# Optimization experiments

Hardware: AMD Instinct MI355X
Metric: run time of the kernel (lower is better)

## Reference

```python
import jax, jax.numpy as jnp
import numpy as np

T, B, E, H = 512, 128, 512, 512
MEM, CTX = 500, 300

def setup_inputs() -> dict:
    key = jax.random.key(0)
    ks = jax.random.split(key, 16)
    s = 0.05
    return {
        "input_seqs": jax.random.normal(ks[0], (B, T, E), jnp.float32),
        "input_lengths": jax.random.randint(ks[1], (B,), 1, T + 1),
        "Wih_f": jax.random.normal(ks[2], (4 * H, E + CTX), jnp.float32) * s,
        "Whh_f": jax.random.normal(ks[3], (4 * H, H), jnp.float32) * s,
        "bih_f": jax.random.normal(ks[4], (4 * H,), jnp.float32) * s,
        "bhh_f": jax.random.normal(ks[5], (4 * H,), jnp.float32) * s,
        "Wih_b": jax.random.normal(ks[6], (4 * H, E + CTX), jnp.float32) * s,
        "Whh_b": jax.random.normal(ks[7], (4 * H, H), jnp.float32) * s,
        "bih_b": jax.random.normal(ks[8], (4 * H,), jnp.float32) * s,
        "bhh_b": jax.random.normal(ks[9], (4 * H,), jnp.float32) * s,
        "Mk_f": jax.random.normal(ks[10], (MEM, H), jnp.float32) * s,
        "Mv_f": jax.random.normal(ks[11], (CTX, MEM), jnp.float32) * s,
        "Mk_b": jax.random.normal(ks[12], (MEM, H), jnp.float32) * s,
        "Mv_b": jax.random.normal(ks[13], (CTX, MEM), jnp.float32) * s,
    }

def _mem_ctx(h, Mk, Mv):
    # exp-key softmax read: exp(h Mk^T) normalized by row sum, then project to CTX
    a = jnp.exp(h @ Mk.T)                      # [B, MEM]
    return (a / jnp.sum(a, axis=-1, keepdims=True)) @ Mv.T  # [B, CTX]

def _cell(x, h, c, Wih, Whh, b):
    g = x @ Wih.T + h @ Whh.T + b              # [B, 4H], gate order i,f,g,o
    i, f, gg, o = jnp.split(g, 4, axis=-1)
    c = jax.nn.sigmoid(f) * c + jax.nn.sigmoid(i) * jnp.tanh(gg)
    return jax.nn.sigmoid(o) * jnp.tanh(c), c

def reference(input_seqs, input_lengths, Wih_f, Whh_f, bih_f, bhh_f,
              Wih_b, Whh_b, bih_b, bhh_b, Mk_f, Mv_f, Mk_b, Mv_b):
    xs = jnp.transpose(input_seqs, (1, 0, 2))          # [T, B, E]
    dt = xs.dtype
    mask = (jnp.arange(T)[:, None] < input_lengths[None, :]).astype(dt)[:, :, None]  # [T,B,1]
    b_f = bih_f + bhh_f
    b_b = bih_b + bhh_b
    z = jnp.zeros((B, H), dt)
    zf = jnp.zeros((), dt)
    one = jnp.ones((), dt)

    def fstep(carry, x):
        h, c, flag = carry
        ctx = flag * _mem_ctx(h, Mk_f, Mv_f)           # step 0 uses zero dummy context
        h, c = _cell(jnp.concatenate([x, ctx], -1), h, c, Wih_f, Whh_f, b_f)
        return (h, c, one), h
    _, f_hs = jax.lax.scan(fstep, (z, z, zf), xs)      # [T, B, H] per-step hidden

    def bstep(carry, xm):
        x, m = xm
        hm, h, c, flag = carry
        ctx = flag * _mem_ctx(hm, Mk_b, Mv_b)
        h, c = _cell(jnp.concatenate([x, ctx], -1), h, c, Wih_b, Whh_b, b_b)
        return (h * m, h, c, one), None                # masked hidden feeds next memory read
    (h_b, _, _, _), _ = jax.lax.scan(bstep, (z, z, z, zf), (xs[::-1], mask[::-1]))

    idx = jnp.clip(input_lengths - 1, 0, T - 1)
    h_f = f_hs[idx, jnp.arange(B)]                     # final valid forward hidden per example
    # permute(1,2,0).view(B,-1): interleave fwd/bwd per hidden unit
    return jnp.stack([h_f, h_b], axis=-1).reshape(B, 2 * H)
```

## Files before the change

### kernel.cpp

```cpp
#include <hip/hip_runtime.h>
#include <hip/hip_bf16.h>

#define T_   512
#define B_   128
#define E_   512
#define H_   512
#define G4_  2048
#define MEM_ 500
#define CTX_ 300
#define EC_  (E_ + CTX_)
#define SPIN_MAX 65536

typedef short sh8  __attribute__((ext_vector_type(8)));
typedef float f32x4 __attribute__((ext_vector_type(4)));

struct ScanParams {
  const float* __restrict__ x;
  const short* __restrict__ xbf;
  const int*   __restrict__ len;
  const float* __restrict__ Wih0; const float* __restrict__ Whh0;
  const float* __restrict__ bih0; const float* __restrict__ bhh0;
  const float* __restrict__ Wih1; const float* __restrict__ Whh1;
  const float* __restrict__ bih1; const float* __restrict__ bhh1;
  const float* __restrict__ Mk0;  const float* __restrict__ Mk1;
  const float* __restrict__ Mf;
  short* __restrict__ hbf;
  short* __restrict__ aB;
  unsigned* __restrict__ bar;
  float* __restrict__ out;
};

__device__ __forceinline__ float sigm_(float x) { return 1.f / (1.f + __expf(-x)); }
__device__ __forceinline__ float tanh_(float x) { return 1.f - 2.f / (__expf(2.f * x) + 1.f); }
__device__ __forceinline__ short f2bs(float f) {
  __hip_bfloat16 h = __float2bfloat16(f);
  short s; __builtin_memcpy(&s, &h, 2); return s;
}
__device__ __forceinline__ float bs2f(short s) {
  unsigned u = ((unsigned)(unsigned short)s) << 16;
  float f; __builtin_memcpy(&f, &u, 4); return f;
}

struct F16 { sh8 v[16]; };
__device__ __forceinline__ void gld16(F16& f, const short* base) {
  asm volatile(
      "global_load_dwordx4 %0, %16, off sc1\n\t"
      "global_load_dwordx4 %1, %16, off offset:64 sc1\n\t"
      "global_load_dwordx4 %2, %16, off offset:128 sc1\n\t"
      "global_load_dwordx4 %3, %16, off offset:192 sc1\n\t"
      "global_load_dwordx4 %4, %16, off offset:256 sc1\n\t"
      "global_load_dwordx4 %5, %16, off offset:320 sc1\n\t"
      "global_load_dwordx4 %6, %16, off offset:384 sc1\n\t"
      "global_load_dwordx4 %7, %16, off offset:448 sc1\n\t"
      "global_load_dwordx4 %8, %16, off offset:512 sc1\n\t"
      "global_load_dwordx4 %9, %16, off offset:576 sc1\n\t"
      "global_load_dwordx4 %10, %16, off offset:640 sc1\n\t"
      "global_load_dwordx4 %11, %16, off offset:704 sc1\n\t"
      "global_load_dwordx4 %12, %16, off offset:768 sc1\n\t"
      "global_load_dwordx4 %13, %16, off offset:832 sc1\n\t"
      "global_load_dwordx4 %14, %16, off offset:896 sc1\n\t"
      "global_load_dwordx4 %15, %16, off offset:960 sc1\n\t"
      "s_waitcnt vmcnt(0)"
      : "=&v"(f.v[0]), "=&v"(f.v[1]), "=&v"(f.v[2]), "=&v"(f.v[3]),
        "=&v"(f.v[4]), "=&v"(f.v[5]), "=&v"(f.v[6]), "=&v"(f.v[7]),
        "=&v"(f.v[8]), "=&v"(f.v[9]), "=&v"(f.v[10]), "=&v"(f.v[11]),
        "=&v"(f.v[12]), "=&v"(f.v[13]), "=&v"(f.v[14]), "=&v"(f.v[15])
      : "v"(base)
      : "memory");
}

__device__ __forceinline__ void st4s(short* base, unsigned d0, unsigned d1,
                                     unsigned d2, unsigned d3) {
  asm volatile(
      "global_store_short %4, %0, off sc1\n\t"
      "global_store_short %4, %1, off offset:1024 sc1\n\t"
      "global_store_short %4, %2, off offset:2048 sc1\n\t"
      "global_store_short %4, %3, off offset:3072 sc1\n\t"
      "s_waitcnt vmcnt(0)"
      :: "v"(d0), "v"(d1), "v"(d2), "v"(d3), "v"(base) : "memory");
}

__device__ __forceinline__ void st8s(short* base, const unsigned* d) {
  asm volatile(
      "global_store_short %8, %0, off sc1\n\t"
      "global_store_short %8, %1, off offset:1024 sc1\n\t"
      "global_store_short %8, %2, off offset:2048 sc1\n\t"
      "global_store_short %8, %3, off offset:3072 sc1\n\t"
      "global_store_short %8, %4, off offset:8 sc1\n\t"
      "global_store_short %8, %5, off offset:1032 sc1\n\t"
      "global_store_short %8, %6, off offset:2056 sc1\n\t"
      "global_store_short %8, %7, off offset:3080 sc1"
      :: "v"(d[0]), "v"(d[1]), "v"(d[2]), "v"(d[3]),
         "v"(d[4]), "v"(d[5]), "v"(d[6]), "v"(d[7]), "v"(base) : "memory");
}

__device__ __forceinline__ bool hchk(const unsigned* hflW, unsigned ep, int lane) {
  unsigned v = __hip_atomic_load(&hflW[lane], __ATOMIC_RELAXED, __HIP_MEMORY_SCOPE_AGENT);
  return __all((int)(v >= ep));
}
__device__ __forceinline__ bool achk(const unsigned* aflW, unsigned ep, int lane) {
  unsigned v = __hip_atomic_load(&aflW[lane & 31], __ATOMIC_RELAXED, __HIP_MEMORY_SCOPE_AGENT);
  return __all((int)(v >= ep));
}
__device__ __forceinline__ void spin_h(const unsigned* hflW, unsigned ep, int lane) {
  int n = 0;
  while (!hchk(hflW, ep, lane) && n < SPIN_MAX) { __builtin_amdgcn_s_sleep(1); ++n; }
}
__device__ __forceinline__ void spin_a(const unsigned* aflW, unsigned ep, int lane) {
  int n = 0;
  while (!achk(aflW, ep, lane) && n < SPIN_MAX) { __builtin_amdgcn_s_sleep(1); ++n; }
}
__device__ __forceinline__ void fset(unsigned* slot, unsigned ep, int lane) {
  if (lane == 0)
    __hip_atomic_store(slot, ep, __ATOMIC_RELAXED, __HIP_MEMORY_SCOPE_AGENT);
}

__global__ __launch_bounds__(256) void xcvt_kernel(const float* __restrict__ x,
                                                   short* __restrict__ xbf) {
  const size_t i = ((size_t)blockIdx.x * 256 + threadIdx.x) * 8;
  f32x4 a = *reinterpret_cast<const f32x4*>(x + i);
  f32x4 b = *reinterpret_cast<const f32x4*>(x + i + 4);
  sh8 v;
  #pragma unroll
  for (int j = 0; j < 4; ++j) { v[j] = f2bs(a[j]); v[4 + j] = f2bs(b[j]); }
  *reinterpret_cast<sh8*>(xbf + i) = v;
}

__global__ __launch_bounds__(256) void mfused_kernel(
    const float* __restrict__ WihF, const float* __restrict__ WihB,
    const float* __restrict__ MvF,  const float* __restrict__ MvB,
    float* __restrict__ Mf) {
  const int d  = blockIdx.x >> 7;
  const int j0 = (blockIdx.x & 127) * 16;
  const float* __restrict__ Wih = d ? WihB : WihF;
  const float* __restrict__ Mv  = d ? MvB  : MvF;
  __shared__ float Wl[16][CTX_ + 1];
  for (int i = threadIdx.x; i < 16 * CTX_; i += 256) {
    int r = i / CTX_, cc = i - r * CTX_;
    Wl[r][cc] = Wih[(size_t)(j0 + r) * EC_ + E_ + cc];
  }
  __syncthreads();
  const int jj = threadIdx.x & 15;
  for (int m = threadIdx.x >> 4; m < MEM_; m += 16) {
    float acc = 0.f;
    for (int cc = 0; cc < CTX_; ++cc)
      acc = fmaf(Mv[cc * MEM_ + m], Wl[jj][cc], acc);
    Mf[(size_t)d * MEM_ * G4_ + (size_t)m * G4_ + j0 + jj] = acc;
  }
}

__global__ __launch_bounds__(512, 1) void scan_kernel(ScanParams p) {
  const int dir  = blockIdx.x >> 6;
  const int w    = blockIdx.x & 63;
  const int tid  = threadIdx.x;
  const int wv   = tid >> 6;
  const int lane = tid & 63;

  __shared__ __align__(16) short WgL[32 * 2 * 64 * 8];
  __shared__ __align__(16) short MkL[16 * 64 * 8];
  __shared__ __align__(16) short MfL[16 * 2 * 64 * 8];
  __shared__ int LvL[B_];

  const float* __restrict__ Wihd = dir ? p.Wih1 : p.Wih0;
  const float* __restrict__ Whhd = dir ? p.Whh1 : p.Whh0;
  const float* __restrict__ bihd = dir ? p.bih1 : p.bih0;
  const float* __restrict__ bhhd = dir ? p.bhh1 : p.bhh0;
  const float* __restrict__ Mkd  = dir ? p.Mk1  : p.Mk0;
  const float* __restrict__ Mfd  = p.Mf + (size_t)dir * MEM_ * G4_;
  short* __restrict__ aBd = p.aB + (size_t)dir * B_ * 512;

  unsigned* __restrict__ hflW = p.bar + (size_t)(dir * 8 + wv) * 64;
  unsigned* __restrict__ aflW = p.bar + 1024 + (size_t)(dir * 8 + wv) * 32;

  const int  ct   = w >> 1;
  const bool prod = ((wv >> 2) == (w & 1));

  for (int i = tid; i < 32 * 2 * 64; i += 512) {
    const int ks = i >> 7, r2 = i & 127, ct2 = r2 >> 6, l2 = r2 & 63;
    const int col = l2 & 15, kg = l2 >> 4;
    const int k0 = ks * 32 + kg * 8;
    const int gc = (col & 3) * H_ + 8 * w + 4 * ct2 + (col >> 2);
    const float* src = (k0 < E_) ? (Wihd + (size_t)gc * EC_ + k0)
                                 : (Whhd + (size_t)gc * H_ + (k0 - E_));
    sh8 v;
    #pragma unroll
    for (int j = 0; j < 8; ++j) v[j] = f2bs(src[j]);
    *reinterpret_cast<sh8*>(&WgL[i * 8]) = v;
  }
  for (int i = tid; i < 16 * 64; i += 512) {
    const int ks = i >> 6, l2 = i & 63;
    const int col = l2 & 15, kg = l2 >> 4;
    const int k0 = ks * 32 + kg * 8;
    const int mr = 16 * ct + col;
    sh8 v;
    #pragma unroll
    for (int j = 0; j < 8; ++j)
      v[j] = (mr < MEM_) ? f2bs(Mkd[(size_t)mr * H_ + k0 + j]) : (short)0;
    *reinterpret_cast<sh8*>(&MkL[i * 8]) = v;
  }
  for (int i = tid; i < 16 * 2 * 64; i += 512) {
    const int ks = i >> 7, r2 = i & 127, ct2 = r2 >> 6, l2 = r2 & 63;
    const int col = l2 & 15, kg = l2 >> 4;
    const int gc = (col & 3) * H_ + 8 * w + 4 * ct2 + (col >> 2);
    const int m0 = ks * 32 + kg * 8;
    sh8 v;
    #pragma unroll
    for (int j = 0; j < 8; ++j)
      v[j] = (m0 + j < MEM_) ? f2bs(Mfd[(size_t)(m0 + j) * G4_ + gc]) : (short)0;
    *reinterpret_cast<sh8*>(&MfL[i * 8]) = v;
  }
  if (tid < B_) LvL[tid] = p.len[tid];

  const int cc  = lane & 15;
  const int q   = cc & 3;
  const int uu  = cc >> 2;
  const int kg8 = (lane >> 4) * 8;
  const int arow = lane & 15;
  float biasl[2];
  #pragma unroll
  for (int ct2 = 0; ct2 < 2; ++ct2) {
    const int gc = q * H_ + 8 * w + 4 * ct2 + uu;
    biasl[ct2] = bihd[gc] + bhhd[gc];
  }

  float creg[2][4] = {{0.f,0.f,0.f,0.f},{0.f,0.f,0.f,0.f}};
  __syncthreads();

  const int mylen = LvL[16 * wv + arow];

  auto xhalf = [&](int t, f32x4* acc) {
    if (p.xbf) {
      const short* xb = p.xbf + ((size_t)(16 * wv + arow) * T_ + t) * E_ + kg8;
      for (int ks = 0; ks < 16; ++ks) {
        sh8 af = *reinterpret_cast<const sh8*>(xb + ks * 32);
        acc[0] = __builtin_amdgcn_mfma_f32_16x16x32_bf16(
            af, *reinterpret_cast<const sh8*>(&WgL[((ks * 2 + 0) * 64 + lane) * 8]), acc[0], 0, 0, 0);
        acc[1] = __builtin_amdgcn_mfma_f32_16x16x32_bf16(
            af, *reinterpret_cast<const sh8*>(&WgL[((ks * 2 + 1) * 64 + lane) * 8]), acc[1], 0, 0, 0);
      }
    } else {
      const float* xp0 = p.x + ((size_t)(16 * wv + arow) * T_ + t) * E_ + kg8;
      for (int ks = 0; ks < 16; ++ks) {
        f32x4 v0 = *reinterpret_cast<const f32x4*>(xp0 + ks * 32);
        f32x4 v1 = *reinterpret_cast<const f32x4*>(xp0 + ks * 32 + 4);
        sh8 af;
        #pragma unroll
        for (int j = 0; j < 4; ++j) { af[j] = f2bs(v0[j]); af[4 + j] = f2bs(v1[j]); }
        acc[0] = __builtin_amdgcn_mfma_f32_16x16x32_bf16(
            af, *reinterpret_cast<const sh8*>(&WgL[((ks * 2 + 0) * 64 + lane) * 8]), acc[0], 0, 0, 0);
        acc[1] = __builtin_amdgcn_mfma_f32_16x16x32_bf16(
            af, *reinterpret_cast<const sh8*>(&WgL[((ks * 2 + 1) * 64 + lane) * 8]), acc[1], 0, 0, 0);
      }
    }
  };

  f32x4 accX[2] = {(f32x4){0,0,0,0}, (f32x4){0,0,0,0}};
  xhalf(dir ? T_ - 1 : 0, accX);

  for (int s = 0; s < T_; ++s) {
    const int t   = dir ? (T_ - 1 - s) : s;
    const int cur = s & 1, prv = cur ^ 1;
    const short* __restrict__ hb_prev = p.hbf + ((size_t)(prv * 2 + dir)) * B_ * H_;
    short*       __restrict__ hb_cur  = p.hbf + ((size_t)(cur * 2 + dir)) * B_ * H_;

    const short* hrow = hb_prev + (size_t)(16 * wv + arow) * H_ + kg8;

    f32x4 accG[2] = { accX[0], accX[1] };

    if (s > 0) spin_h(hflW, (unsigned)s, lane);
    __builtin_amdgcn_sched_barrier(0);
    F16 fH;
    gld16(fH, hrow);

    if (prod) {
      f32x4 accA = (f32x4){0, 0, 0, 0};
      const sh8 z8 = (sh8){0,0,0,0,0,0,0,0};
      const bool keep = !dir || ((t + 1) < mylen);
      for (int ks = 0; ks < 16; ++ks) {
        sh8 af = keep ? fH.v[ks] : z8;
        accA = __builtin_amdgcn_mfma_f32_16x16x32_bf16(
            af, *reinterpret_cast<const sh8*>(&MkL[(ks * 64 + lane) * 8]), accA, 0, 0, 0);
      }
      const int m = 16 * ct + arow;
      unsigned d[4];
      #pragma unroll
      for (int r = 0; r < 4; ++r) {
        float e = (m < MEM_) ? __expf(accA[r]) : 0.f;
        d[r] = (unsigned)(unsigned short)f2bs(e);
      }
      st4s(aBd + (size_t)(16 * wv + 4 * (lane >> 4)) * 512 + m, d[0], d[1], d[2], d[3]);
      fset(&aflW[ct], (unsigned)(s + 1), lane);
    }

    for (int ks = 0; ks < 16; ++ks) {
      accG[0] = __builtin_amdgcn_mfma_f32_16x16x32_bf16(
          fH.v[ks], *reinterpret_cast<const sh8*>(&WgL[(((16 + ks) * 2 + 0) * 64 + lane) * 8]), accG[0], 0, 0, 0);
      accG[1] = __builtin_amdgcn_mfma_f32_16x16x32_bf16(
          fH.v[ks], *reinterpret_cast<const sh8*>(&WgL[(((16 + ks) * 2 + 1) * 64 + lane) * 8]), accG[1], 0, 0, 0);
    }

    accX[0] = (f32x4){0,0,0,0}; accX[1] = (f32x4){0,0,0,0};
    if (s + 1 < T_) xhalf(dir ? (T_ - 2 - s) : (s + 1), accX);

    f32x4 accC[2] = {(f32x4){0,0,0,0}, (f32x4){0,0,0,0}};
    float inv4[4] = {0.f, 0.f, 0.f, 0.f};
    if (s > 0) {
      spin_a(aflW, (unsigned)(s + 1), lane);
      __builtin_amdgcn_sched_barrier(0);
      F16 fC;
      gld16(fC, aBd + (size_t)(16 * wv + arow) * 512 + kg8);
      float rs = 0.f;
      for (int ks = 0; ks < 16; ++ks) {
        accC[0] = __builtin_amdgcn_mfma_f32_16x16x32_bf16(
            fC.v[ks], *reinterpret_cast<const sh8*>(&MfL[((ks * 2 + 0) * 64 + lane) * 8]), accC[0], 0, 0, 0);
        accC[1] = __builtin_amdgcn_mfma_f32_16x16x32_bf16(
            fC.v[ks], *reinterpret_cast<const sh8*>(&MfL[((ks * 2 + 1) * 64 + lane) * 8]), accC[1], 0, 0, 0);
        #pragma unroll
        for (int j = 0; j < 8; ++j) rs += bs2f(fC.v[ks][j]);
      }
      rs += __shfl_xor(rs, 16);
      rs += __shfl_xor(rs, 32);
      #pragma unroll
      for (int r = 0; r < 4; ++r)
        inv4[r] = 1.f / __shfl(rs, 4 * (lane >> 4) + r);
    }

    unsigned hsd[8]; float hvv[2][4];
    #pragma unroll
    for (int ct2 = 0; ct2 < 2; ++ct2) {
      float g4[4];
      #pragma unroll
      for (int r = 0; r < 4; ++r) {
        float v = accG[ct2][r] + biasl[ct2];
        if (s > 0) v += accC[ct2][r] * inv4[r];
        g4[r] = v;
      }
      #pragma unroll
      for (int r = 0; r < 4; ++r) {
        const float x1 = __shfl_xor(g4[r], 1);
        const float x2 = __shfl_xor(g4[r], 2);
        const float x3 = __shfl_xor(g4[r], 3);
        const float iv = (q==0)?g4[r]:(q==1)?x1:(q==2)?x2:x3;
        const float fv = (q==0)?x1:(q==1)?g4[r]:(q==2)?x3:x2;
        const float gv = (q==0)?x2:(q==1)?x3:(q==2)?g4[r]:x1;
        const float ov = (q==0)?x3:(q==1)?x2:(q==2)?x1:g4[r];
        float cv = creg[ct2][r];
        cv = sigm_(fv) * cv + sigm_(iv) * tanh_(gv);
        const float hv = sigm_(ov) * tanh_(cv);
        creg[ct2][r] = cv;
        hvv[ct2][r] = hv;
        hsd[ct2 * 4 + r] = (unsigned)(unsigned short)f2bs(hv);
      }
    }
    if (q == 0) {
      const int b0 = 16 * wv + 4 * (lane >> 4);
      const int unit0 = 8 * w + uu;
      unsigned hord[8] = {hsd[0],hsd[1],hsd[2],hsd[3],hsd[4],hsd[5],hsd[6],hsd[7]};
      st8s(hb_cur + (size_t)b0 * H_ + unit0, hord);
      #pragma unroll
      for (int ct2 = 0; ct2 < 2; ++ct2) {
        #pragma unroll
        for (int r = 0; r < 4; ++r) {
          const int b = b0 + r;
          const int unit = unit0 + 4 * ct2;
          if (dir == 0) {
            if (t == LvL[b] - 1) p.out[b * (2 * H_) + 2 * unit] = hvv[ct2][r];
          } else {
            if (s == T_ - 1) p.out[b * (2 * H_) + 2 * unit + 1] = hvv[ct2][r];
          }
        }
      }
    }
    asm volatile("s_waitcnt vmcnt(0)" ::: "memory");
    fset(&hflW[w], (unsigned)(s + 1), lane);
  }
}

extern "C" void kernel_launch(void* const* d_in, const int* in_sizes, int n_in,
                              void* d_out, int out_size, void* d_ws, size_t ws_size,
                              hipStream_t stream) {
  (void)in_sizes; (void)n_in; (void)out_size;

  ScanParams p;
  p.x    = (const float*)d_in[0];
  p.len  = (const int*)  d_in[1];
  p.Wih0 = (const float*)d_in[2];
  p.Whh0 = (const float*)d_in[3];
  p.bih0 = (const float*)d_in[4];
  p.bhh0 = (const float*)d_in[5];
  p.Wih1 = (const float*)d_in[6];
  p.Whh1 = (const float*)d_in[7];
  p.bih1 = (const float*)d_in[8];
  p.bhh1 = (const float*)d_in[9];
  p.Mk0  = (const float*)d_in[10];
  const float* MvF = (const float*)d_in[11];
  p.Mk1  = (const float*)d_in[12];
  const float* MvB = (const float*)d_in[13];

  char* ws = (char*)d_ws;
  size_t off = 0;
  auto alloc = [&](size_t bytes) -> void* {
    void* ptr = ws + off; off += (bytes + 255) & ~(size_t)255; return ptr;
  };
  float*    Mf   = (float*)   alloc((size_t)2 * MEM_ * G4_ * 4);
  short*    hbf  = (short*)   alloc((size_t)2 * 2 * B_ * H_ * 2);
  short*    aB   = (short*)   alloc((size_t)2 * B_ * 512 * 2);
  unsigned* bar  = (unsigned*)alloc((size_t)1536 * sizeof(unsigned));
  size_t xbf_off = off;
  short*    xbf  = (short*)   alloc((size_t)B_ * T_ * E_ * 2);
  const bool useXbf = (ws_size >= xbf_off + (size_t)B_ * T_ * E_ * 2);

  p.Mf = Mf; p.hbf = hbf; p.aB = aB; p.bar = bar;
  p.xbf = useXbf ? xbf : nullptr;
  p.out = (float*)d_out;

  hipMemsetAsync(hbf, 0, (size_t)2 * 2 * B_ * H_ * 2, stream);
  hipMemsetAsync(bar, 0, (size_t)1536 * sizeof(unsigned), stream);

  if (useXbf) {
    const size_t n8 = (size_t)B_ * T_ * E_ / 8;
    xcvt_kernel<<<dim3((unsigned)(n8 / 256)), dim3(256), 0, stream>>>(p.x, xbf);
  }
  mfused_kernel<<<dim3(256), dim3(256), 0, stream>>>(
      (const float*)d_in[2], (const float*)d_in[6], MvF, MvB, Mf);

  void* args[] = { &p };
  hipLaunchCooperativeKernel((const void*)scan_kernel, dim3(128), dim3(512),
                             args, 0, stream);
}
```

Measured before the change: 9.385 ms.

## Replace flag-based barriers with tagged data words polled directly by consumers

Each bf16 hidden and attention value is now stored in a 32-bit word with the step index packed into the low half. Consumers repeatedly load the data and check the tags instead of spinning on separate flag arrays and then reloading. This removes the store-drain wait, the flag write and the extra round trip per step. In exchange the exchanged buffers double in size, each poll reloads full fragments and must unpack them, and correctness depends on 32-bit stores being seen atomically.

```diff
diff --git a/kernel.cpp b/kernel.cpp
--- a/kernel.cpp
+++ b/kernel.cpp
@@ -13,6 +13,7 @@
 
 typedef short sh8  __attribute__((ext_vector_type(8)));
 typedef float f32x4 __attribute__((ext_vector_type(4)));
+typedef unsigned u32x4 __attribute__((ext_vector_type(4)));
 
 struct ScanParams {
   const float* __restrict__ x;
@@ -24,9 +25,8 @@
   const float* __restrict__ bih1; const float* __restrict__ bhh1;
   const float* __restrict__ Mk0;  const float* __restrict__ Mk1;
   const float* __restrict__ Mf;
-  short* __restrict__ hbf;
-  short* __restrict__ aB;
-  unsigned* __restrict__ bar;
+  unsigned* __restrict__ hbU;
+  unsigned* __restrict__ aBU;
   float* __restrict__ out;
 };
 
@@ -41,25 +41,25 @@
   float f; __builtin_memcpy(&f, &u, 4); return f;
 }
 
-struct F16 { sh8 v[16]; };
-__device__ __forceinline__ void gld16(F16& f, const short* base) {
+struct R16 { u32x4 v[16]; };
+__device__ __forceinline__ void gld16p(R16& f, const unsigned* base) {
   asm volatile(
       "global_load_dwordx4 %0, %16, off sc1\n\t"
-      "global_load_dwordx4 %1, %16, off offset:64 sc1\n\t"
+      "global_load_dwordx4 %1, %16, off offset:16 sc1\n\t"
       "global_load_dwordx4 %2, %16, off offset:128 sc1\n\t"
-      "global_load_dwordx4 %3, %16, off offset:192 sc1\n\t"
+      "global_load_dwordx4 %3, %16, off offset:144 sc1\n\t"
       "global_load_dwordx4 %4, %16, off offset:256 sc1\n\t"
-      "global_load_dwordx4 %5, %16, off offset:320 sc1\n\t"
+      "global_load_dwordx4 %5, %16, off offset:272 sc1\n\t"
       "global_load_dwordx4 %6, %16, off offset:384 sc1\n\t"
-      "global_load_dwordx4 %7, %16, off offset:448 sc1\n\t"
+      "global_load_dwordx4 %7, %16, off offset:400 sc1\n\t"
       "global_load_dwordx4 %8, %16, off offset:512 sc1\n\t"
-      "global_load_dwordx4 %9, %16, off offset:576 sc1\n\t"
+      "global_load_dwordx4 %9, %16, off offset:528 sc1\n\t"
       "global_load_dwordx4 %10, %16, off offset:640 sc1\n\t"
-      "global_load_dwordx4 %11, %16, off offset:704 sc1\n\t"
+      "global_load_dwordx4 %11, %16, off offset:656 sc1\n\t"
       "global_load_dwordx4 %12, %16, off offset:768 sc1\n\t"
-      "global_load_dwordx4 %13, %16, off offset:832 sc1\n\t"
+      "global_load_dwordx4 %13, %16, off offset:784 sc1\n\t"
       "global_load_dwordx4 %14, %16, off offset:896 sc1\n\t"
-      "global_load_dwordx4 %15, %16, off offset:960 sc1\n\t"
+      "global_load_dwordx4 %15, %16, off offset:912 sc1\n\t"
       "s_waitcnt vmcnt(0)"
       : "=&v"(f.v[0]), "=&v"(f.v[1]), "=&v"(f.v[2]), "=&v"(f.v[3]),
         "=&v"(f.v[4]), "=&v"(f.v[5]), "=&v"(f.v[6]), "=&v"(f.v[7]),
@@ -69,50 +69,48 @@
       : "memory");
 }
 
-__device__ __forceinline__ void st4s(short* base, unsigned d0, unsigned d1,
-                                     unsigned d2, unsigned d3) {
+__device__ __forceinline__ unsigned vr8(const R16& r, unsigned tag, sh8* frag) {
+  unsigned bad = 0;
+  #pragma unroll
+  for (int k = 0; k < 8; ++k) {
+    u32x4 a = r.v[2 * k], b = r.v[2 * k + 1];
+    #pragma unroll
+    for (int j = 0; j < 4; ++j) {
+      bad |= (a[j] & 0xffffu) ^ tag;
+      bad |= (b[j] & 0xffffu) ^ tag;
+    }
+    u32x4 d;
+    d[0] = (a[0] >> 16) | (a[1] & 0xffff0000u);
+    d[1] = (a[2] >> 16) | (a[3] & 0xffff0000u);
+    d[2] = (b[0] >> 16) | (b[1] & 0xffff0000u);
+    d[3] = (b[2] >> 16) | (b[3] & 0xffff0000u);
+    frag[k] = *reinterpret_cast<sh8*>(&d);
+  }
+  return bad;
+}
+
+__device__ __forceinline__ void st4d(unsigned* b01, unsigned* b23,
+                                     unsigned d0, unsigned d1, unsigned d2, unsigned d3) {
   asm volatile(
-      "global_store_short %4, %0, off sc1\n\t"
-      "global_store_short %4, %1, off offset:1024 sc1\n\t"
-      "global_store_short %4, %2, off offset:2048 sc1\n\t"
-      "global_store_short %4, %3, off offset:3072 sc1\n\t"
-      "s_waitcnt vmcnt(0)"
-      :: "v"(d0), "v"(d1), "v"(d2), "v"(d3), "v"(base) : "memory");
-}
-
-__device__ __forceinline__ void st8s(short* base, const unsigned* d) {
+      "global_store_dword %4, %0, off sc1\n\t"
+      "global_store_dword %4, %1, off offset:2048 sc1\n\t"
+      "global_store_dword %5, %2, off sc1\n\t"
+      "global_store_dword %5, %3, off offset:2048 sc1"
+      :: "v"(d0), "v"(d1), "v"(d2), "v"(d3), "v"(b01), "v"(b23) : "memory");
+}
+
+__device__ __forceinline__ void st8d(unsigned* b01, unsigned* b23, const unsigned* d) {
   asm volatile(
-      "global_store_short %8, %0, off sc1\n\t"
-      "global_store_short %8, %1, off offset:1024 sc1\n\t"
-      "global_store_short %8, %2, off offset:2048 sc1\n\t"
-      "global_store_short %8, %3, off offset:3072 sc1\n\t"
-      "global_store_short %8, %4, off offset:8 sc1\n\t"
-      "global_store_short %8, %5, off offset:1032 sc1\n\t"
-      "global_store_short %8, %6, off offset:2056 sc1\n\t"
-      "global_store_short %8, %7, off offset:3080 sc1"
+      "global_store_dword %8, %0, off sc1\n\t"
+      "global_store_dword %8, %1, off offset:2048 sc1\n\t"
+      "global_store_dword %9, %2, off sc1\n\t"
+      "global_store_dword %9, %3, off offset:2048 sc1\n\t"
+      "global_store_dword %8, %4, off offset:16 sc1\n\t"
+      "global_store_dword %8, %5, off offset:2064 sc1\n\t"
+      "global_store_dword %9, %6, off offset:16 sc1\n\t"
+      "global_store_dword %9, %7, off offset:2064 sc1"
       :: "v"(d[0]), "v"(d[1]), "v"(d[2]), "v"(d[3]),
-         "v"(d[4]), "v"(d[5]), "v"(d[6]), "v"(d[7]), "v"(base) : "memory");
-}
-
-__device__ __forceinline__ bool hchk(const unsigned* hflW, unsigned ep, int lane) {
-  unsigned v = __hip_atomic_load(&hflW[lane], __ATOMIC_RELAXED, __HIP_MEMORY_SCOPE_AGENT);
-  return __all((int)(v >= ep));
-}
-__device__ __forceinline__ bool achk(const unsigned* aflW, unsigned ep, int lane) {
-  unsigned v = __hip_atomic_load(&aflW[lane & 31], __ATOMIC_RELAXED, __HIP_MEMORY_SCOPE_AGENT);
-  return __all((int)(v >= ep));
-}
-__device__ __forceinline__ void spin_h(const unsigned* hflW, unsigned ep, int lane) {
-  int n = 0;
-  while (!hchk(hflW, ep, lane) && n < SPIN_MAX) { __builtin_amdgcn_s_sleep(1); ++n; }
-}
-__device__ __forceinline__ void spin_a(const unsigned* aflW, unsigned ep, int lane) {
-  int n = 0;
-  while (!achk(aflW, ep, lane) && n < SPIN_MAX) { __builtin_amdgcn_s_sleep(1); ++n; }
-}
-__device__ __forceinline__ void fset(unsigned* slot, unsigned ep, int lane) {
-  if (lane == 0)
-    __hip_atomic_store(slot, ep, __ATOMIC_RELAXED, __HIP_MEMORY_SCOPE_AGENT);
+         "v"(d[4]), "v"(d[5]), "v"(d[6]), "v"(d[7]), "v"(b01), "v"(b23) : "memory");
 }
 
 __global__ __launch_bounds__(256) void xcvt_kernel(const float* __restrict__ x,
@@ -167,10 +165,7 @@
   const float* __restrict__ bhhd = dir ? p.bhh1 : p.bhh0;
   const float* __restrict__ Mkd  = dir ? p.Mk1  : p.Mk0;
   const float* __restrict__ Mfd  = p.Mf + (size_t)dir * MEM_ * G4_;
-  short* __restrict__ aBd = p.aB + (size_t)dir * B_ * 512;
-
-  unsigned* __restrict__ hflW = p.bar + (size_t)(dir * 8 + wv) * 64;
-  unsigned* __restrict__ aflW = p.bar + 1024 + (size_t)(dir * 8 + wv) * 32;
+  unsigned* __restrict__ aBU_d = p.aBU + (size_t)dir * B_ * 512;
 
   const int  ct   = w >> 1;
   const bool prod = ((wv >> 2) == (w & 1));
@@ -214,7 +209,8 @@
   const int cc  = lane & 15;
   const int q   = cc & 3;
   const int uu  = cc >> 2;
-  const int kg8 = (lane >> 4) * 8;
+  const int g2  = lane >> 4;
+  const int kg8 = g2 * 8;
   const int arow = lane & 15;
   float biasl[2];
   #pragma unroll
@@ -227,6 +223,17 @@
   __syncthreads();
 
   const int mylen = LvL[16 * wv + arow];
+
+  auto poll16 = [&](const unsigned* base, unsigned tag, sh8* frag) {
+    R16 r;
+    int n = 0;
+    for (;;) {
+      gld16p(r, base);
+      unsigned bad = vr8(r, tag, frag);
+      if (__all((int)(bad == 0)) || n >= SPIN_MAX) break;
+      __builtin_amdgcn_s_sleep(1); ++n;
+    }
+  };
 
   auto xhalf = [&](int t, f32x4* acc) {
     if (p.xbf) {
@@ -260,24 +267,28 @@
   for (int s = 0; s < T_; ++s) {
     const int t   = dir ? (T_ - 1 - s) : s;
     const int cur = s & 1, prv = cur ^ 1;
-    const short* __restrict__ hb_prev = p.hbf + ((size_t)(prv * 2 + dir)) * B_ * H_;
-    short*       __restrict__ hb_cur  = p.hbf + ((size_t)(cur * 2 + dir)) * B_ * H_;
-
-    const short* hrow = hb_prev + (size_t)(16 * wv + arow) * H_ + kg8;
+    const unsigned* __restrict__ hb_prevU = p.hbU + ((size_t)(prv * 2 + dir)) * B_ * H_;
+    unsigned*       __restrict__ hb_curU  = p.hbU + ((size_t)(cur * 2 + dir)) * B_ * H_;
+
+    const unsigned tagH = (unsigned)s;
+    const unsigned tagW = (unsigned)(s + 1);
 
     f32x4 accG[2] = { accX[0], accX[1] };
 
-    if (s > 0) spin_h(hflW, (unsigned)s, lane);
-    __builtin_amdgcn_sched_barrier(0);
-    F16 fH;
-    gld16(fH, hrow);
+    sh8 fHf[16];
+    {
+      const unsigned* hbase = hb_prevU + (size_t)(16 * wv + arow) * 512 + kg8;
+      poll16(hbase,       tagH, &fHf[0]);
+      poll16(hbase + 256, tagH, &fHf[8]);
+    }
 
     if (prod) {
       f32x4 accA = (f32x4){0, 0, 0, 0};
       const sh8 z8 = (sh8){0,0,0,0,0,0,0,0};
       const bool keep = !dir || ((t + 1) < mylen);
+      #pragma unroll
       for (int ks = 0; ks < 16; ++ks) {
-        sh8 af = keep ? fH.v[ks] : z8;
+        sh8 af = keep ? fHf[ks] : z8;
         accA = __builtin_amdgcn_mfma_f32_16x16x32_bf16(
             af, *reinterpret_cast<const sh8*>(&MkL[(ks * 64 + lane) * 8]), accA, 0, 0, 0);
       }
@@ -286,17 +297,18 @@
       #pragma unroll
       for (int r = 0; r < 4; ++r) {
         float e = (m < MEM_) ? __expf(accA[r]) : 0.f;
-        d[r] = (unsigned)(unsigned short)f2bs(e);
-      }
-      st4s(aBd + (size_t)(16 * wv + 4 * (lane >> 4)) * 512 + m, d[0], d[1], d[2], d[3]);
-      fset(&aflW[ct], (unsigned)(s + 1), lane);
-    }
-
+        d[r] = ((unsigned)(unsigned short)f2bs(e) << 16) | tagW;
+      }
+      unsigned* ab01 = aBU_d + (size_t)(16 * wv + 4 * g2) * 512 + m;
+      st4d(ab01, ab01 + 1024, d[0], d[1], d[2], d[3]);
+    }
+
+    #pragma unroll
     for (int ks = 0; ks < 16; ++ks) {
       accG[0] = __builtin_amdgcn_mfma_f32_16x16x32_bf16(
-          fH.v[ks], *reinterpret_cast<const sh8*>(&WgL[(((16 + ks) * 2 + 0) * 64 + lane) * 8]), accG[0], 0, 0, 0);
+          fHf[ks], *reinterpret_cast<const sh8*>(&WgL[(((16 + ks) * 2 + 0) * 64 + lane) * 8]), accG[0], 0, 0, 0);
       accG[1] = __builtin_amdgcn_mfma_f32_16x16x32_bf16(
-          fH.v[ks], *reinterpret_cast<const sh8*>(&WgL[(((16 + ks) * 2 + 1) * 64 + lane) * 8]), accG[1], 0, 0, 0);
+          fHf[ks], *reinterpret_cast<const sh8*>(&WgL[(((16 + ks) * 2 + 1) * 64 + lane) * 8]), accG[1], 0, 0, 0);
     }
 
     accX[0] = (f32x4){0,0,0,0}; accX[1] = (f32x4){0,0,0,0};
@@ -305,24 +317,28 @@
     f32x4 accC[2] = {(f32x4){0,0,0,0}, (f32x4){0,0,0,0}};
     float inv4[4] = {0.f, 0.f, 0.f, 0.f};
     if (s > 0) {
-      spin_a(aflW, (unsigned)(s + 1), lane);
-      __builtin_amdgcn_sched_barrier(0);
-      F16 fC;
-      gld16(fC, aBd + (size_t)(16 * wv + arow) * 512 + kg8);
       float rs = 0.f;
-      for (int ks = 0; ks < 16; ++ks) {
-        accC[0] = __builtin_amdgcn_mfma_f32_16x16x32_bf16(
-            fC.v[ks], *reinterpret_cast<const sh8*>(&MfL[((ks * 2 + 0) * 64 + lane) * 8]), accC[0], 0, 0, 0);
-        accC[1] = __builtin_amdgcn_mfma_f32_16x16x32_bf16(
-            fC.v[ks], *reinterpret_cast<const sh8*>(&MfL[((ks * 2 + 1) * 64 + lane) * 8]), accC[1], 0, 0, 0);
+      const unsigned* cb = aBU_d + (size_t)(16 * wv + arow) * 512 + kg8;
+      #pragma unroll
+      for (int c = 0; c < 2; ++c) {
+        sh8 fCf[8];
+        poll16(cb + 256 * c, tagW, fCf);
         #pragma unroll
-        for (int j = 0; j < 8; ++j) rs += bs2f(fC.v[ks][j]);
+        for (int k = 0; k < 8; ++k) {
+          const int ks = 8 * c + k;
+          accC[0] = __builtin_amdgcn_mfma_f32_16x16x32_bf16(
+              fCf[k], *reinterpret_cast<const sh8*>(&MfL[((ks * 2 + 0) * 64 + lane) * 8]), accC[0], 0, 0, 0);
+          accC[1] = __builtin_amdgcn_mfma_f32_16x16x32_bf16(
+              fCf[k], *reinterpret_cast<const sh8*>(&MfL[((ks * 2 + 1) * 64 + lane) * 8]), accC[1], 0, 0, 0);
+          #pragma unroll
+          for (int j = 0; j < 8; ++j) rs += bs2f(fCf[k][j]);
+        }
       }
       rs += __shfl_xor(rs, 16);
       rs += __shfl_xor(rs, 32);
       #pragma unroll
       for (int r = 0; r < 4; ++r)
-        inv4[r] = 1.f / __shfl(rs, 4 * (lane >> 4) + r);
+        inv4[r] = 1.f / __shfl(rs, 4 * g2 + r);
     }
 
     unsigned hsd[8]; float hvv[2][4];
@@ -349,14 +365,15 @@
         const float hv = sigm_(ov) * tanh_(cv);
         creg[ct2][r] = cv;
         hvv[ct2][r] = hv;
-        hsd[ct2 * 4 + r] = (unsigned)(unsigned short)f2bs(hv);
+        hsd[ct2 * 4 + r] = ((unsigned)(unsigned short)f2bs(hv) << 16) | tagW;
       }
     }
     if (q == 0) {
-      const int b0 = 16 * wv + 4 * (lane >> 4);
+      const int b0 = 16 * wv + 4 * g2;
       const int unit0 = 8 * w + uu;
+      unsigned* hb01 = hb_curU + (size_t)b0 * 512 + unit0;
       unsigned hord[8] = {hsd[0],hsd[1],hsd[2],hsd[3],hsd[4],hsd[5],hsd[6],hsd[7]};
-      st8s(hb_cur + (size_t)b0 * H_ + unit0, hord);
+      st8d(hb01, hb01 + 1024, hord);
       #pragma unroll
       for (int ct2 = 0; ct2 < 2; ++ct2) {
         #pragma unroll
@@ -371,8 +388,6 @@
         }
       }
     }
-    asm volatile("s_waitcnt vmcnt(0)" ::: "memory");
-    fset(&hflW[w], (unsigned)(s + 1), lane);
   }
 }
 
@@ -402,20 +417,18 @@
   auto alloc = [&](size_t bytes) -> void* {
     void* ptr = ws + off; off += (bytes + 255) & ~(size_t)255; return ptr;
   };
-  float*    Mf   = (float*)   alloc((size_t)2 * MEM_ * G4_ * 4);
-  short*    hbf  = (short*)   alloc((size_t)2 * 2 * B_ * H_ * 2);
-  short*    aB   = (short*)   alloc((size_t)2 * B_ * 512 * 2);
-  unsigned* bar  = (unsigned*)alloc((size_t)1536 * sizeof(unsigned));
+  float*    Mf  = (float*)   alloc((size_t)2 * MEM_ * G4_ * 4);
+  unsigned* hbU = (unsigned*)alloc((size_t)2 * 2 * B_ * H_ * 4);
+  unsigned* aBU = (unsigned*)alloc((size_t)2 * B_ * 512 * 4);
   size_t xbf_off = off;
-  short*    xbf  = (short*)   alloc((size_t)B_ * T_ * E_ * 2);
+  short*    xbf = (short*)   alloc((size_t)B_ * T_ * E_ * 2);
   const bool useXbf = (ws_size >= xbf_off + (size_t)B_ * T_ * E_ * 2);
 
-  p.Mf = Mf; p.hbf = hbf; p.aB = aB; p.bar = bar;
+  p.Mf = Mf; p.hbU = hbU; p.aBU = aBU;
   p.xbf = useXbf ? xbf : nullptr;
   p.out = (float*)d_out;
 
-  hipMemsetAsync(hbf, 0, (size_t)2 * 2 * B_ * H_ * 2, stream);
-  hipMemsetAsync(bar, 0, (size_t)1536 * sizeof(unsigned), stream);
+  hipMemsetAsync(hbU, 0, (size_t)2 * 2 * B_ * H_ * 4 + (size_t)2 * B_ * 512 * 4, stream);
 
   if (useXbf) {
     const size_t n8 = (size_t)B_ * T_ * E_ / 8;
```

Result: slower. 14.69 ms (+56.5%).
